# Kernel tuning notes

Hardware: AMD Instinct MI355X
Metric: run time of the kernel (lower is better)

## Reference

```python
import jax, jax.numpy as jnp
import numpy as np

POS_KL_W = 0.1
NEG_KL_W = 0.02
ORDER_W = 0.5
N_BINS = 1000
SIGMA = 0.1
EPS = 1e-09


def setup_inputs() -> dict:
    key = jax.random.key(0)
    k1, k2, k3 = jax.random.split(key, 3)
    N, D, C = 256, 512, 16
    T_F = jax.random.normal(k1, (N, D), dtype=jnp.float32)
    S_F = jax.random.normal(k2, (N, D), dtype=jnp.float32)
    labels = jax.random.uniform(k3, (N, C), dtype=jnp.float32)  # argmax -> class ids
    return {"T_F": T_F, "S_F": S_F, "labels": labels}


def _histograms_and_means(x, pos_labels, neg_labels, t):
    # x: [N, D]; L2-normalize rows (eps matches F.normalize default 1e-12)
    norm = jnp.maximum(jnp.linalg.norm(x, axis=-1, keepdims=True), 1e-12)
    xn = x / norm
    cos = xn @ xn.T                      # [N, N]
    dists = cos.reshape(-1)              # [N*N]
    # Gaussian soft-binning: [N*N, N_BINS] (the big memory-bound intermediate)
    delta = jnp.exp(-0.5 * ((dists[:, None] - t[None, :]) / SIGMA) ** 2)
    neg_w = neg_labels.reshape(-1)
    pos_w = pos_labels.reshape(-1)
    neg_p = (neg_w @ delta) / jnp.sum(neg_w)   # [N_BINS]
    pos_p = (pos_w @ delta) / jnp.sum(pos_w)   # [N_BINS]
    E_pos = jnp.sum(cos * pos_labels, axis=-1) / jnp.sum(pos_labels, axis=-1)  # [N]
    E_neg = jnp.sum(cos * neg_labels, axis=-1) / jnp.sum(neg_labels, axis=-1)  # [N]
    return neg_p, pos_p, E_neg, E_pos


def _kl(anchor, dist):
    # torch F.kl_div(log(dist+eps), anchor+eps, reduction='batchmean'); batch dim is 1
    a = anchor + EPS
    d = dist + EPS
    return jnp.sum(a * (jnp.log(a) - jnp.log(d)))


def reference(T_F, S_F, labels):
    N = T_F.shape[0]
    t = jnp.arange(-1.0, 1.0, 2.0 / N_BINS, dtype=jnp.float32)  # [1000] bin centers
    lab = jnp.argmax(labels, axis=-1)                            # [N]
    grid = (lab[None, :] == lab[:, None]).astype(jnp.float32)    # [N, N]
    neg_labels = 1.0 - grid
    pos_labels = grid * (1.0 - jnp.eye(N, dtype=jnp.float32))

    neg_t, pos_t, E_neg_t, E_pos_t = _histograms_and_means(T_F, pos_labels, neg_labels, t)
    neg_s, pos_s, E_neg_s, E_pos_s = _histograms_and_means(S_F, pos_labels, neg_labels, t)

    pos_kl = POS_KL_W * _kl(pos_t, pos_s)
    neg_kl = NEG_KL_W * _kl(neg_t, neg_s)
    o1 = jnp.mean(jnp.abs(E_pos_t - E_pos_s))
    o2 = jnp.mean(jnp.abs(E_neg_t - E_neg_s))
    o3 = jnp.mean(E_pos_s - E_neg_s)
    order_loss = ORDER_W * (o1 + o2 + o3)
    return pos_kl + neg_kl + order_loss
```

## Files before the change

### kernel.cpp

```cpp
#include <hip/hip_runtime.h>
#include <math.h>

#define N 256
#define D 512
#define C 16
#define NBINS 1000
#define MCELL 1000
#define MSTRIDE 1024
#define EPSF 1e-9f
#define KEXP2 -72.134752f
#define TAILB 64

__device__ inline float waveReduceSum(float v) {
#pragma unroll
    for (int off = 32; off > 0; off >>= 1) v += __shfl_down(v, off, 64);
    return v;
}
__device__ inline double waveReduceSumD(double v) {
#pragma unroll
    for (int off = 32; off > 0; off >>= 1) v += __shfl_down(v, off, 64);
    return v;
}

__global__ void k_prep(const float* __restrict__ labels, int* __restrict__ lab,
                       float* __restrict__ mg, unsigned int* __restrict__ cnt) {
    int b = blockIdx.x;
    int tid = threadIdx.x;
    if (b < 12) {
        ((float4*)mg)[b * 256 + tid] = make_float4(0.f, 0.f, 0.f, 0.f);
    } else {
        if (tid == 0) cnt[0] = 0u;
        float best = labels[tid * C];
        int bi = 0;
#pragma unroll
        for (int c = 1; c < C; ++c) {
            float v = labels[tid * C + c];
            if (v > best) { best = v; bi = c; }
        }
        lab[tid] = bi;
    }
}

__global__ void __launch_bounds__(256) k_main(
        const float* __restrict__ T, const float* __restrict__ S,
        const int* __restrict__ lab, float* __restrict__ mg,
        float* __restrict__ Earr, float* __restrict__ cpos) {
    int mat = blockIdx.y;
    int i0 = blockIdx.x * 2;
    int j = threadIdx.x;
    const float* X = mat ? S : T;
    __shared__ float rowA[D], rowB[D];
    __shared__ float invs[256];
    __shared__ float mom[6 * MSTRIDE];
    __shared__ float red[4][6];
    for (int i = j; i < 6 * MSTRIDE; i += 256) mom[i] = 0.f;
    rowA[j] = X[i0 * D + j];
    rowA[j + 256] = X[i0 * D + 256 + j];
    rowB[j] = X[(i0 + 1) * D + j];
    rowB[j + 256] = X[(i0 + 1) * D + 256 + j];
    __syncthreads();

    float d0 = 0.f, d1 = 0.f, ssq = 0.f;
    {
        const float4* xrow = (const float4*)(X + (size_t)j * D);
        const float4* rA4 = (const float4*)rowA;
        const float4* rB4 = (const float4*)rowB;
#pragma unroll 16
        for (int k4 = 0; k4 < 128; ++k4) {
            float4 xj = xrow[k4];
            float4 a4 = rA4[k4];
            float4 b4 = rB4[k4];
            d0 = fmaf(a4.x, xj.x, fmaf(a4.y, xj.y, fmaf(a4.z, xj.z, fmaf(a4.w, xj.w, d0))));
            d1 = fmaf(b4.x, xj.x, fmaf(b4.y, xj.y, fmaf(b4.z, xj.z, fmaf(b4.w, xj.w, d1))));
            ssq = fmaf(xj.x, xj.x, fmaf(xj.y, xj.y, fmaf(xj.z, xj.z, fmaf(xj.w, xj.w, ssq))));
        }
    }
    invs[j] = 1.0f / fmaxf(sqrtf(ssq), 1e-12f);
    __syncthreads();
    float invj = invs[j];
    float av0 = d0 * invs[i0] * invj;
    float av1 = d1 * invs[i0 + 1] * invj;

    int labj = lab[j];
    bool diag0 = (j == i0), diag1 = (j == i0 + 1);
    float wp0 = (labj == lab[i0] && !diag0) ? 1.f : 0.f;
    float wp1 = (labj == lab[i0 + 1] && !diag1) ? 1.f : 0.f;

    if (!diag0) {
        int jc = (int)floorf((av0 + 1.f) * 500.f);
        jc = max(0, min(jc, MCELL - 1));
        float del = av0 - (-1.f + ((float)jc + 0.5f) * 0.002f);
        float dd = del * del;
        atomicAdd(&mom[jc], 1.f);
        atomicAdd(&mom[MSTRIDE + jc], del);
        atomicAdd(&mom[2 * MSTRIDE + jc], dd);
        if (wp0 > 0.f) {
            atomicAdd(&mom[3 * MSTRIDE + jc], 1.f);
            atomicAdd(&mom[4 * MSTRIDE + jc], del);
            atomicAdd(&mom[5 * MSTRIDE + jc], dd);
        }
    }
    if (!diag1) {
        int jc = (int)floorf((av1 + 1.f) * 500.f);
        jc = max(0, min(jc, MCELL - 1));
        float del = av1 - (-1.f + ((float)jc + 0.5f) * 0.002f);
        float dd = del * del;
        atomicAdd(&mom[jc], 1.f);
        atomicAdd(&mom[MSTRIDE + jc], del);
        atomicAdd(&mom[2 * MSTRIDE + jc], dd);
        if (wp1 > 0.f) {
            atomicAdd(&mom[3 * MSTRIDE + jc], 1.f);
            atomicAdd(&mom[4 * MSTRIDE + jc], del);
            atomicAdd(&mom[5 * MSTRIDE + jc], dd);
        }
    }

    float r0 = waveReduceSum(diag0 ? 0.f : av0);
    float r1 = waveReduceSum(av0 * wp0);
    float r2 = waveReduceSum(wp0);
    float r3 = waveReduceSum(diag1 ? 0.f : av1);
    float r4 = waveReduceSum(av1 * wp1);
    float r5 = waveReduceSum(wp1);
    int wid = j >> 6, lane = j & 63;
    if (lane == 0) {
        red[wid][0] = r0; red[wid][1] = r1; red[wid][2] = r2;
        red[wid][3] = r3; red[wid][4] = r4; red[wid][5] = r5;
    }
    __syncthreads();
    if (j < 2) {
        float sA = 0, sP = 0, cP = 0;
        for (int w = 0; w < 4; ++w) {
            sA += red[w][j * 3 + 0];
            sP += red[w][j * 3 + 1];
            cP += red[w][j * 3 + 2];
        }
        int row = i0 + j;
        Earr[(mat * 2 + 0) * N + row] = sP / cP;
        Earr[(mat * 2 + 1) * N + row] = (sA - sP) / (255.f - cP);
        if (mat == 0) cpos[row] = cP;
    }
    for (int i = j; i < 6 * MSTRIDE; i += 256) {
        float v = mom[i];
        if (v != 0.f) atomicAdd(&mg[mat * 6144 + i], v);
    }
}

__global__ void __launch_bounds__(256) k_tail(const float* __restrict__ mg,
                                              const float* __restrict__ Earr,
                                              const float* __restrict__ cpos,
                                              float* __restrict__ pkl,
                                              unsigned int* __restrict__ cnt,
                                              float* __restrict__ out) {
    int b = blockIdx.x;
    int tid = threadIdx.x;
    int wid = tid >> 6, lane = tid & 63;
    __shared__ float sm[12288];
    __shared__ float binres[16][4];
    __shared__ float kterm[16][2];
    __shared__ float credL[4];
    __shared__ unsigned int old_s;
    __shared__ double dred[4][5];

    for (int i = tid; i < 3072; i += 256)
        ((float4*)sm)[i] = ((const float4*)mg)[i];

    float cv = cpos[tid];
    cv = waveReduceSum(cv);
    if (lane == 0) credL[wid] = cv;
    __syncthreads();
    float pcnt = credL[0] + credL[1] + credL[2] + credL[3];
    float ncnt = 65280.f - pcnt;

    int u = tid >> 4, sub = tid & 15;
    int bin = b * 16 + u;
    float t = -1.f + 0.002f * (float)bin;
    float paT = 0.f, saT = 0.f, paS = 0.f, saS = 0.f;
    for (int c = sub; c < MCELL; c += 16) {
        float m0T = sm[c], m0S = sm[6144 + c];
        if (m0T == 0.f && m0S == 0.f) continue;
        float cj = -1.f + ((float)c + 0.5f) * 0.002f;
        float q = cj - t;
        float q2 = q * q;
        if (q2 < 0.5f) {
            float E = __builtin_amdgcn_exp2f(KEXP2 * q2);
            float u1 = 100.f * q;
            float w2 = fmaf(0.5f * u1, u1, -50.f);
            saT = fmaf(E, fmaf(w2, sm[2048 + c], fmaf(-u1, sm[1024 + c], m0T)), saT);
            paT = fmaf(E, fmaf(w2, sm[5120 + c], fmaf(-u1, sm[4096 + c], sm[3072 + c])), paT);
            saS = fmaf(E, fmaf(w2, sm[6144 + 2048 + c], fmaf(-u1, sm[6144 + 1024 + c], m0S)), saS);
            paS = fmaf(E, fmaf(w2, sm[6144 + 5120 + c], fmaf(-u1, sm[6144 + 4096 + c], sm[6144 + 3072 + c])), paS);
        }
    }
#pragma unroll
    for (int off = 1; off < 16; off <<= 1) {
        paT += __shfl_xor(paT, off, 16);
        saT += __shfl_xor(saT, off, 16);
        paS += __shfl_xor(paS, off, 16);
        saS += __shfl_xor(saS, off, 16);
    }
    if (sub == 0) {
        binres[u][0] = paT; binres[u][1] = saT;
        binres[u][2] = paS; binres[u][3] = saS;
    }
    __syncthreads();

    if (tid < 16) {
        int bn = b * 16 + tid;
        float pk = 0.f, nk = 0.f;
        if (bn < NBINS) {
            float hpT = binres[tid][0], hsT = binres[tid][1];
            float hpS = binres[tid][2], hsS = binres[tid][3];
            float pt = hpT / pcnt;
            float nt = (hsT - hpT) / ncnt;
            float ps = hpS / pcnt;
            float ns = (hsS - hpS) / ncnt;
            pk = (pt + EPSF) * (__logf(pt + EPSF) - __logf(ps + EPSF));
            nk = (nt + EPSF) * (__logf(nt + EPSF) - __logf(ns + EPSF));
        }
        kterm[tid][0] = pk;
        kterm[tid][1] = nk;
    }
    __syncthreads();
    if (tid == 0) {
        float a = 0.f, bb = 0.f;
        for (int q = 0; q < 16; ++q) { a += kterm[q][0]; bb += kterm[q][1]; }
        pkl[b * 2] = a;
        pkl[b * 2 + 1] = bb;
        __threadfence();
        old_s = atomicAdd(cnt, 1u);
    }
    __syncthreads();
    if (old_s != TAILB - 1) return;

    __threadfence();
    double a = 0.0, bb = 0.0;
    if (tid < TAILB) {
        volatile const float* vp = pkl;
        a = (double)vp[2 * tid];
        bb = (double)vp[2 * tid + 1];
    }
    a = waveReduceSumD(a);
    bb = waveReduceSumD(bb);
    double o1, o2, o3;
    {
        float ept = Earr[0 * N + tid];
        float ent = Earr[1 * N + tid];
        float eps_ = Earr[2 * N + tid];
        float ens = Earr[3 * N + tid];
        o1 = fabs((double)ept - (double)eps_);
        o2 = fabs((double)ent - (double)ens);
        o3 = (double)eps_ - (double)ens;
    }
    o1 = waveReduceSumD(o1);
    o2 = waveReduceSumD(o2);
    o3 = waveReduceSumD(o3);
    if (lane == 0) {
        dred[wid][0] = a;  dred[wid][1] = bb;
        dred[wid][2] = o1; dred[wid][3] = o2; dred[wid][4] = o3;
    }
    __syncthreads();
    if (tid == 0) {
        double A = dred[0][0], B = dred[0][1];
        double Co = 0, Do = 0, Eo = 0;
        for (int w = 0; w < 4; ++w) {
            Co += dred[w][2]; Do += dred[w][3]; Eo += dred[w][4];
        }
        double loss = 0.1 * A + 0.02 * B + 0.5 * ((Co + Do + Eo) / (double)N);
        out[0] = (float)loss;
    }
}

extern "C" void kernel_launch(void* const* d_in, const int* in_sizes, int n_in,
                              void* d_out, int out_size, void* d_ws, size_t ws_size,
                              hipStream_t stream) {
    const float* T = (const float*)d_in[0];
    const float* S = (const float*)d_in[1];
    const float* labels = (const float*)d_in[2];
    float* out = (float*)d_out;

    float* ws = (float*)d_ws;
    float* mg = ws;
    float* Earr = mg + 12288;
    float* cpos = Earr + 1024;
    float* pkl = cpos + 256;
    unsigned int* cnt = (unsigned int*)(pkl + 128);
    int* lab = (int*)(cnt + 1);

    k_prep<<<13, 256, 0, stream>>>(labels, lab, mg, cnt);
    k_main<<<dim3(N / 2, 2), 256, 0, stream>>>(T, S, lab, mg, Earr, cpos);
    k_tail<<<TAILB, 256, 0, stream>>>(mg, Earr, cpos, pkl, cnt, out);
}
```

Measured before the change: 48.22 us.

## Compute four rows per block with split-K over two thread halves

Each block of k_main now handles four query rows instead of two and runs 512 threads. The two halves of the block each take half of the D dimension and combine their partial dot products through shared memory. This halves the number of blocks, and with them the per-block global atomic flushes of the 6x1024 moment histogram and the re-reads of X. In exchange it adds a shared-memory partial-sum exchange and an extra barrier, and leaves fewer blocks to spread across the GPU.

```diff
diff --git a/kernel.cpp b/kernel.cpp
--- a/kernel.cpp
+++ b/kernel.cpp
@@ -41,105 +41,119 @@
     }
 }
 
-__global__ void __launch_bounds__(256) k_main(
+__global__ void __launch_bounds__(512) k_main(
         const float* __restrict__ T, const float* __restrict__ S,
         const int* __restrict__ lab, float* __restrict__ mg,
         float* __restrict__ Earr, float* __restrict__ cpos) {
     int mat = blockIdx.y;
-    int i0 = blockIdx.x * 2;
-    int j = threadIdx.x;
+    int i0 = blockIdx.x * 4;
+    int t = threadIdx.x;
+    int h = t >> 8, jj = t & 255;
     const float* X = mat ? S : T;
-    __shared__ float rowA[D], rowB[D];
+
+    __shared__ float rows[4 * D];
+    __shared__ float psum[5][512];
     __shared__ float invs[256];
     __shared__ float mom[6 * MSTRIDE];
-    __shared__ float red[4][6];
-    for (int i = j; i < 6 * MSTRIDE; i += 256) mom[i] = 0.f;
-    rowA[j] = X[i0 * D + j];
-    rowA[j + 256] = X[i0 * D + 256 + j];
-    rowB[j] = X[(i0 + 1) * D + j];
-    rowB[j + 256] = X[(i0 + 1) * D + 256 + j];
-    __syncthreads();
-
-    float d0 = 0.f, d1 = 0.f, ssq = 0.f;
+    __shared__ float red[8][6];
+
+    for (int i = t; i < 6 * MSTRIDE; i += 512) mom[i] = 0.f;
+#pragma unroll
+    for (int f = t; f < 4 * D; f += 512) rows[f] = X[i0 * D + f];
+    __syncthreads();
+
+    float d0 = 0.f, d1 = 0.f, d2 = 0.f, d3 = 0.f, ssq = 0.f;
     {
-        const float4* xrow = (const float4*)(X + (size_t)j * D);
-        const float4* rA4 = (const float4*)rowA;
-        const float4* rB4 = (const float4*)rowB;
-#pragma unroll 16
-        for (int k4 = 0; k4 < 128; ++k4) {
+        const float4* xrow = (const float4*)(X + (size_t)jj * D + h * 256);
+        const float4* r0 = (const float4*)(rows + 0 * D + h * 256);
+        const float4* r1 = (const float4*)(rows + 1 * D + h * 256);
+        const float4* r2 = (const float4*)(rows + 2 * D + h * 256);
+        const float4* r3 = (const float4*)(rows + 3 * D + h * 256);
+#pragma unroll 8
+        for (int k4 = 0; k4 < 64; ++k4) {
             float4 xj = xrow[k4];
-            float4 a4 = rA4[k4];
-            float4 b4 = rB4[k4];
-            d0 = fmaf(a4.x, xj.x, fmaf(a4.y, xj.y, fmaf(a4.z, xj.z, fmaf(a4.w, xj.w, d0))));
-            d1 = fmaf(b4.x, xj.x, fmaf(b4.y, xj.y, fmaf(b4.z, xj.z, fmaf(b4.w, xj.w, d1))));
+            float4 a = r0[k4];
+            float4 b = r1[k4];
+            float4 c = r2[k4];
+            float4 e = r3[k4];
+            d0 = fmaf(a.x, xj.x, fmaf(a.y, xj.y, fmaf(a.z, xj.z, fmaf(a.w, xj.w, d0))));
+            d1 = fmaf(b.x, xj.x, fmaf(b.y, xj.y, fmaf(b.z, xj.z, fmaf(b.w, xj.w, d1))));
+            d2 = fmaf(c.x, xj.x, fmaf(c.y, xj.y, fmaf(c.z, xj.z, fmaf(c.w, xj.w, d2))));
+            d3 = fmaf(e.x, xj.x, fmaf(e.y, xj.y, fmaf(e.z, xj.z, fmaf(e.w, xj.w, d3))));
             ssq = fmaf(xj.x, xj.x, fmaf(xj.y, xj.y, fmaf(xj.z, xj.z, fmaf(xj.w, xj.w, ssq))));
         }
     }
-    invs[j] = 1.0f / fmaxf(sqrtf(ssq), 1e-12f);
-    __syncthreads();
-    float invj = invs[j];
-    float av0 = d0 * invs[i0] * invj;
-    float av1 = d1 * invs[i0 + 1] * invj;
-
-    int labj = lab[j];
-    bool diag0 = (j == i0), diag1 = (j == i0 + 1);
-    float wp0 = (labj == lab[i0] && !diag0) ? 1.f : 0.f;
-    float wp1 = (labj == lab[i0 + 1] && !diag1) ? 1.f : 0.f;
-
-    if (!diag0) {
-        int jc = (int)floorf((av0 + 1.f) * 500.f);
-        jc = max(0, min(jc, MCELL - 1));
-        float del = av0 - (-1.f + ((float)jc + 0.5f) * 0.002f);
-        float dd = del * del;
-        atomicAdd(&mom[jc], 1.f);
-        atomicAdd(&mom[MSTRIDE + jc], del);
-        atomicAdd(&mom[2 * MSTRIDE + jc], dd);
-        if (wp0 > 0.f) {
-            atomicAdd(&mom[3 * MSTRIDE + jc], 1.f);
-            atomicAdd(&mom[4 * MSTRIDE + jc], del);
-            atomicAdd(&mom[5 * MSTRIDE + jc], dd);
-        }
-    }
-    if (!diag1) {
-        int jc = (int)floorf((av1 + 1.f) * 500.f);
-        jc = max(0, min(jc, MCELL - 1));
-        float del = av1 - (-1.f + ((float)jc + 0.5f) * 0.002f);
-        float dd = del * del;
-        atomicAdd(&mom[jc], 1.f);
-        atomicAdd(&mom[MSTRIDE + jc], del);
-        atomicAdd(&mom[2 * MSTRIDE + jc], dd);
-        if (wp1 > 0.f) {
-            atomicAdd(&mom[3 * MSTRIDE + jc], 1.f);
-            atomicAdd(&mom[4 * MSTRIDE + jc], del);
-            atomicAdd(&mom[5 * MSTRIDE + jc], dd);
-        }
-    }
-
-    float r0 = waveReduceSum(diag0 ? 0.f : av0);
-    float r1 = waveReduceSum(av0 * wp0);
-    float r2 = waveReduceSum(wp0);
-    float r3 = waveReduceSum(diag1 ? 0.f : av1);
-    float r4 = waveReduceSum(av1 * wp1);
-    float r5 = waveReduceSum(wp1);
-    int wid = j >> 6, lane = j & 63;
-    if (lane == 0) {
-        red[wid][0] = r0; red[wid][1] = r1; red[wid][2] = r2;
-        red[wid][3] = r3; red[wid][4] = r4; red[wid][5] = r5;
-    }
-    __syncthreads();
-    if (j < 2) {
+    psum[0][t] = d0; psum[1][t] = d1; psum[2][t] = d2; psum[3][t] = d3;
+    psum[4][t] = ssq;
+    __syncthreads();
+    if (t < 256) {
+        float sq = psum[4][t] + psum[4][t + 256];
+        invs[t] = 1.0f / fmaxf(sqrtf(sq), 1e-12f);
+    }
+    __syncthreads();
+
+    float invj = invs[jj];
+    float av[4];
+#pragma unroll
+    for (int r = 0; r < 4; ++r)
+        av[r] = (psum[r][jj] + psum[r][jj + 256]) * invs[i0 + r] * invj;
+
+    int labj = lab[jj];
+    float wp[4];
+#pragma unroll
+    for (int r = 0; r < 4; ++r)
+        wp[r] = (labj == lab[i0 + r] && jj != i0 + r) ? 1.f : 0.f;
+
+#pragma unroll
+    for (int rr = 0; rr < 2; ++rr) {
+        int r = h * 2 + rr;
+        if (jj != i0 + r) {
+            float d = av[r];
+            int jc = (int)floorf((d + 1.f) * 500.f);
+            jc = max(0, min(jc, MCELL - 1));
+            float del = d - (-1.f + ((float)jc + 0.5f) * 0.002f);
+            float dd = del * del;
+            atomicAdd(&mom[jc], 1.f);
+            atomicAdd(&mom[MSTRIDE + jc], del);
+            atomicAdd(&mom[2 * MSTRIDE + jc], dd);
+            if (wp[r] > 0.f) {
+                atomicAdd(&mom[3 * MSTRIDE + jc], 1.f);
+                atomicAdd(&mom[4 * MSTRIDE + jc], del);
+                atomicAdd(&mom[5 * MSTRIDE + jc], dd);
+            }
+        }
+    }
+
+    {
+        int rA = h * 2, rB = h * 2 + 1;
+        float r0v = waveReduceSum((jj != i0 + rA) ? av[rA] : 0.f);
+        float r1v = waveReduceSum(av[rA] * wp[rA]);
+        float r2v = waveReduceSum(wp[rA]);
+        float r3v = waveReduceSum((jj != i0 + rB) ? av[rB] : 0.f);
+        float r4v = waveReduceSum(av[rB] * wp[rB]);
+        float r5v = waveReduceSum(wp[rB]);
+        int wid = t >> 6, lane = t & 63;
+        if (lane == 0) {
+            red[wid][0] = r0v; red[wid][1] = r1v; red[wid][2] = r2v;
+            red[wid][3] = r3v; red[wid][4] = r4v; red[wid][5] = r5v;
+        }
+    }
+    __syncthreads();
+    if (t < 4) {
+        int wb = (t >> 1) * 4;
+        int sel = (t & 1) * 3;
         float sA = 0, sP = 0, cP = 0;
         for (int w = 0; w < 4; ++w) {
-            sA += red[w][j * 3 + 0];
-            sP += red[w][j * 3 + 1];
-            cP += red[w][j * 3 + 2];
-        }
-        int row = i0 + j;
+            sA += red[wb + w][sel + 0];
+            sP += red[wb + w][sel + 1];
+            cP += red[wb + w][sel + 2];
+        }
+        int row = i0 + t;
         Earr[(mat * 2 + 0) * N + row] = sP / cP;
         Earr[(mat * 2 + 1) * N + row] = (sA - sP) / (255.f - cP);
         if (mat == 0) cpos[row] = cP;
     }
-    for (int i = j; i < 6 * MSTRIDE; i += 256) {
+    for (int i = t; i < 6 * MSTRIDE; i += 512) {
         float v = mom[i];
         if (v != 0.f) atomicAdd(&mg[mat * 6144 + i], v);
     }
@@ -287,6 +301,6 @@
     int* lab = (int*)(cnt + 1);
 
     k_prep<<<13, 256, 0, stream>>>(labels, lab, mg, cnt);
-    k_main<<<dim3(N / 2, 2), 256, 0, stream>>>(T, S, lab, mg, Earr, cpos);
+    k_main<<<dim3(N / 4, 2), 512, 0, stream>>>(T, S, lab, mg, Earr, cpos);
     k_tail<<<TAILB, 256, 0, stream>>>(mg, Earr, cpos, pkl, cnt, out);
 }
```

Measured after the change: 48.13 us (median of 2 runs). No clear change (-0.2%).
